# Optimization experiments

Measured on AMD Instinct MI355X. Metric: run time of the kernel, lower is better.

Reference implementation:

```python
import jax, jax.numpy as jnp
import numpy as np

HS = [192, 96, 48, 24, 12, 6]
WS = [384, 192, 96, 48, 24, 12]
C = 64    # feature channels per pyramid level
F = 64    # num_features (conv output channels)
CIN = 2 * C + 2  # current + warped + 2 flow channels = 130
N = 4


def dense_image_warp(image, flow):
    """tfa.image.dense_image_warp: warped[b,y,x] = bilinear(image[b, y - flow_y, x - flow_x]).
    Boundary handling matches tfa._interpolate_bilinear: floor indices clipped to
    [0, size-2], interpolation alphas clipped to [0, 1]."""
    n, h, w, _ = image.shape
    gy, gx = jnp.meshgrid(jnp.arange(h, dtype=flow.dtype),
                          jnp.arange(w, dtype=flow.dtype), indexing='ij')
    qy = gy[None] - flow[..., 0]          # [N,H,W] query rows
    qx = gx[None] - flow[..., 1]          # [N,H,W] query cols
    y0 = jnp.clip(jnp.floor(qy), 0, h - 2).astype(jnp.int32)
    x0 = jnp.clip(jnp.floor(qx), 0, w - 2).astype(jnp.int32)
    ay = jnp.clip(qy - y0.astype(flow.dtype), 0.0, 1.0)[..., None]
    ax = jnp.clip(qx - x0.astype(flow.dtype), 0.0, 1.0)[..., None]
    b = jnp.arange(n)[:, None, None]
    tl = image[b, y0, x0]
    tr = image[b, y0, x0 + 1]
    bl = image[b, y0 + 1, x0]
    br = image[b, y0 + 1, x0 + 1]
    top = tl + (tr - tl) * ax
    bot = bl + (br - bl) * ax
    return top + (bot - top) * ay


def separable_conv1x1(x, dw, pw, bias):
    # SeparableConv2D with 1x1 kernel: depthwise per-channel scale, then pointwise matmul.
    return jnp.einsum('nhwc,cf->nhwf', x * dw, pw) + bias


def _forward(xcs, xps, fls, dws, pws, bs):
    outs = []
    for i in range(6):
        # _warp: dense_image_warp(x_prev, -flow)
        warped = dense_image_warp(xps[i], -fls[i])
        x = jnp.concatenate([xcs[i], warped, fls[i]], axis=-1)  # [N,H,W,130]
        outs.append(separable_conv1x1(x, dws[i], pws[i], bs[i]))
    return tuple(outs)


def setup_inputs() -> dict:
    key = jax.random.key(0)
    d = {}
    for i in range(6):
        h, w = HS[i], WS[i]
        ks = jax.random.split(jax.random.fold_in(key, i), 6)
        d[f'xc{i}'] = jax.random.normal(ks[0], (N, h, w, C), jnp.float32)
        d[f'xp{i}'] = jax.random.normal(ks[1], (N, h, w, C), jnp.float32)
        d[f'fl{i}'] = jax.random.normal(ks[2], (N, h, w, 2), jnp.float32) * 2.0
        d[f'dw{i}'] = jax.random.normal(ks[3], (CIN,), jnp.float32) * 0.1
        d[f'pw{i}'] = jax.random.normal(ks[4], (CIN, F), jnp.float32) * 0.05
        d[f'bias{i}'] = jnp.zeros((F,), jnp.float32)
    return d


def reference(xc0, xc1, xc2, xc3, xc4, xc5,
              xp0, xp1, xp2, xp3, xp4, xp5,
              fl0, fl1, fl2, fl3, fl4, fl5,
              dw0, dw1, dw2, dw3, dw4, dw5,
              pw0, pw1, pw2, pw3, pw4, pw5,
              bias0, bias1, bias2, bias3, bias4, bias5):
    xcs = (xc0, xc1, xc2, xc3, xc4, xc5)
    xps = (xp0, xp1, xp2, xp3, xp4, xp5)
    fls = (fl0, fl1, fl2, fl3, fl4, fl5)
    dws = (dw0, dw1, dw2, dw3, dw4, dw5)
    pws = (pw0, pw1, pw2, pw3, pw4, pw5)
    bs = (bias0, bias1, bias2, bias3, bias4, bias5)
    return _forward(xcs, xps, fls, dws, pws, bs)
```

## Files before the change

kernel.cpp:

```cpp
#include <hip/hip_runtime.h>


typedef __attribute__((ext_vector_type(8))) short bf16x8;
typedef __attribute__((ext_vector_type(4))) float f32x4;

#define WS_LVL_STRIDE 17408

__device__ inline unsigned rne_bf16_bits(float f) {
  unsigned u = __builtin_bit_cast(unsigned, f);
  u += 0x7fffu + ((u >> 16) & 1u);
  return u >> 16;
}
__device__ inline int pack_bf16x2(float a, float b) {
  return (int)(rne_bf16_bits(a) | (rne_bf16_bits(b) << 16));
}

struct LevelArgs {
  const float* __restrict__ xc;
  const float* __restrict__ xp;
  const float* __restrict__ fl;
  float* __restrict__ out;
  const char* __restrict__ wsl;
  int H, W, npix, block_start;
};
struct KArgs { LevelArgs lv[6]; int total_blocks; };

struct PrepLevel {
  const float* __restrict__ dw;
  const float* __restrict__ pw;
  const float* __restrict__ bias;
  char* __restrict__ wsl;
};
struct PrepArgs { PrepLevel lv[6]; };

__global__ void prep_kernel(PrepArgs pa) {
  const PrepLevel P = pa.lv[blockIdx.x];
  int4* __restrict__ frag = (int4*)P.wsl;
  for (int e = (int)threadIdx.x; e < 1024; e += 256) {
    const int kt = e >> 8;
    const int nt = (e >> 6) & 3;
    const int lane = e & 63;
    const int n = nt * 16 + (lane & 15);
    const int kb = kt * 32 + ((lane >> 4) & 3) * 8;
    int v[4];
#pragma unroll
    for (int jj = 0; jj < 4; ++jj) {
      const int k0 = kb + jj * 2;
      const float w0 = P.dw[k0] * P.pw[(size_t)k0 * 64 + n];
      const float w1 = P.dw[k0 + 1] * P.pw[(size_t)(k0 + 1) * 64 + n];
      v[jj] = pack_bf16x2(w0, w1);
    }
    frag[e] = make_int4(v[0], v[1], v[2], v[3]);
  }
  float* __restrict__ tab = (float*)(P.wsl + 16384);
  if (threadIdx.x < 64) {
    const int f = (int)threadIdx.x;
    tab[f] = P.bias[f];
    tab[64 + f] = P.dw[128] * P.pw[128 * 64 + f];
    tab[128 + f] = P.dw[129] * P.pw[129 * 64 + f];
  }
}

#define LDS_ROW 144
#define LDS_FL_OFF (256 * LDS_ROW)

__global__ __launch_bounds__(256, 3) void flowwarp_mfma(KArgs ka) {
  __shared__ __align__(16) char lds_raw[256 * LDS_ROW + 256 * 8];

  const int nb = ka.total_blocks;
  const int chunk = (nb + 7) >> 3;
  const int bp = (int)blockIdx.x;
  const int b = (bp & 7) * chunk + (bp >> 3);
  if (b >= nb) return;

  int Lr = 0;
#pragma unroll
  for (int i = 1; i < 6; ++i) Lr = (b >= ka.lv[i].block_start) ? i : Lr;
  const int L = __builtin_amdgcn_readfirstlane(Lr);
  const LevelArgs A = ka.lv[L];

  const int q = (int)threadIdx.x;
  const int p0 = (b - A.block_start) * 256;
  const int W = A.W, H = A.H;

  {
    int p = p0 + q;
    if (p > A.npix - 1) p = A.npix - 1;
    const int x = p % W;
    const int t = p / W;
    const int y = t % H;
    const int n = t / H;

    const float fl0 = A.fl[2 * (size_t)p];
    const float fl1 = A.fl[2 * (size_t)p + 1];
    ((float2*)(lds_raw + LDS_FL_OFF))[q] = make_float2(fl0, fl1);

    const float qy = (float)y + fl0;
    const float qx = (float)x + fl1;
    const float fy = fminf(fmaxf(floorf(qy), 0.0f), (float)(H - 2));
    const float fx = fminf(fmaxf(floorf(qx), 0.0f), (float)(W - 2));
    const int y0 = (int)fy, x0 = (int)fx;
    const float ay = fminf(fmaxf(qy - fy, 0.0f), 1.0f);
    const float ax = fminf(fmaxf(qx - fx, 0.0f), 1.0f);

    const float* __restrict__ base =
        A.xp + ((size_t)((n * H + y0) * W + x0)) * 64;
    const int W64 = W * 64;
    const float4* __restrict__ tl4 = (const float4*)base;
    const float4* __restrict__ tr4 = (const float4*)(base + 64);
    const float4* __restrict__ bl4 = (const float4*)(base + W64);
    const float4* __restrict__ br4 = (const float4*)(base + W64 + 64);
    int4* __restrict__ xrow = (int4*)(lds_raw + (size_t)q * LDS_ROW);

#pragma unroll 1
    for (int bq = 0; bq < 4; ++bq) {
      float4 rtl[4], rtr[4], rbl[4], rbr[4];
#pragma unroll
      for (int i = 0; i < 4; ++i) {
        rtl[i] = tl4[bq * 4 + i];
        rtr[i] = tr4[bq * 4 + i];
        rbl[i] = bl4[bq * 4 + i];
        rbr[i] = br4[bq * 4 + i];
      }
      int v[8];
#pragma unroll
      for (int i = 0; i < 4; ++i) {
        const float atl[4] = {rtl[i].x, rtl[i].y, rtl[i].z, rtl[i].w};
        const float atr[4] = {rtr[i].x, rtr[i].y, rtr[i].z, rtr[i].w};
        const float abl[4] = {rbl[i].x, rbl[i].y, rbl[i].z, rbl[i].w};
        const float abr[4] = {rbr[i].x, rbr[i].y, rbr[i].z, rbr[i].w};
        float wv[4];
#pragma unroll
        for (int j = 0; j < 4; ++j) {
          const float top = fmaf(atr[j] - atl[j], ax, atl[j]);
          const float bot = fmaf(abr[j] - abl[j], ax, abl[j]);
          wv[j] = fmaf(bot - top, ay, top);
        }
        v[i * 2] = pack_bf16x2(wv[0], wv[1]);
        v[i * 2 + 1] = pack_bf16x2(wv[2], wv[3]);
      }
      xrow[bq * 2] = make_int4(v[0], v[1], v[2], v[3]);
      xrow[bq * 2 + 1] = make_int4(v[4], v[5], v[6], v[7]);
    }
  }
  __syncthreads();

  const int lane = q & 63;
  const int w = q >> 6;
  const int m16 = lane & 15;
  const int q4l = lane >> 4;

  const int4* __restrict__ bfr = (const int4*)A.wsl;
  bf16x8 Bf[4][4];
#pragma unroll
  for (int kt = 0; kt < 4; ++kt)
#pragma unroll
    for (int nt = 0; nt < 4; ++nt)
      Bf[kt][nt] = __builtin_bit_cast(bf16x8, bfr[(kt * 4 + nt) * 64 + lane]);

  const float* __restrict__ tab = (const float*)(A.wsl + 16384);
  float bv[4], t0v[4], t1v[4];
#pragma unroll
  for (int nt = 0; nt < 4; ++nt) {
    const int col = nt * 16 + m16;
    bv[nt] = tab[col];
    t0v[nt] = tab[64 + col];
    t1v[nt] = tab[128 + col];
  }
  const float2* __restrict__ flsh = (const float2*)(lds_raw + LDS_FL_OFF);

#pragma unroll 1
  for (int mt = 0; mt < 4; ++mt) {
    const int lrow = w * 64 + mt * 16;
    int pm = p0 + lrow + m16;
    if (pm > A.npix - 1) pm = A.npix - 1;
    const float* __restrict__ xcp = A.xc + (size_t)pm * 64 + q4l * 8;
    const float4 a0 = *(const float4*)xcp;
    const float4 a1 = *(const float4*)(xcp + 4);
    const float4 a2 = *(const float4*)(xcp + 32);
    const float4 a3 = *(const float4*)(xcp + 36);
    int av[8];
    av[0] = pack_bf16x2(a0.x, a0.y); av[1] = pack_bf16x2(a0.z, a0.w);
    av[2] = pack_bf16x2(a1.x, a1.y); av[3] = pack_bf16x2(a1.z, a1.w);
    av[4] = pack_bf16x2(a2.x, a2.y); av[5] = pack_bf16x2(a2.z, a2.w);
    av[6] = pack_bf16x2(a3.x, a3.y); av[7] = pack_bf16x2(a3.z, a3.w);
    const bf16x8 A0 = __builtin_bit_cast(bf16x8, make_int4(av[0], av[1], av[2], av[3]));
    const bf16x8 A1 = __builtin_bit_cast(bf16x8, make_int4(av[4], av[5], av[6], av[7]));
    const int4* __restrict__ lrp =
        (const int4*)(lds_raw + (size_t)(lrow + m16) * LDS_ROW + q4l * 16);
    const bf16x8 A2 = __builtin_bit_cast(bf16x8, lrp[0]);
    const bf16x8 A3 = __builtin_bit_cast(bf16x8, lrp[4]);

    f32x4 acc[4] = {{0.f, 0.f, 0.f, 0.f}, {0.f, 0.f, 0.f, 0.f},
                    {0.f, 0.f, 0.f, 0.f}, {0.f, 0.f, 0.f, 0.f}};
#pragma unroll
    for (int nt = 0; nt < 4; ++nt) {
      acc[nt] = __builtin_amdgcn_mfma_f32_16x16x32_bf16(A0, Bf[0][nt], acc[nt], 0, 0, 0);
      acc[nt] = __builtin_amdgcn_mfma_f32_16x16x32_bf16(A1, Bf[1][nt], acc[nt], 0, 0, 0);
      acc[nt] = __builtin_amdgcn_mfma_f32_16x16x32_bf16(A2, Bf[2][nt], acc[nt], 0, 0, 0);
      acc[nt] = __builtin_amdgcn_mfma_f32_16x16x32_bf16(A3, Bf[3][nt], acc[nt], 0, 0, 0);
    }

    float f0[4], f1[4];
#pragma unroll
    for (int i = 0; i < 4; ++i) {
      const float2 f = flsh[lrow + q4l * 4 + i];
      f0[i] = f.x; f1[i] = f.y;
    }
#pragma unroll
    for (int i = 0; i < 4; ++i) {
      const int prow = p0 + lrow + q4l * 4 + i;
      if (prow < A.npix) {
        float* __restrict__ orow = A.out + (size_t)prow * 64 + m16;
#pragma unroll
        for (int nt = 0; nt < 4; ++nt)
          orow[nt * 16] = acc[nt][i] + bv[nt] + f0[i] * t0v[nt] + f1[i] * t1v[nt];
      }
    }
  }
}

extern "C" void kernel_launch(void* const* d_in, const int* in_sizes, int n_in,
                              void* d_out, int out_size, void* d_ws, size_t ws_size,
                              hipStream_t stream) {
  static const int HS[6] = {192, 96, 48, 24, 12, 6};
  static const int WS[6] = {384, 192, 96, 48, 24, 12};
  PrepArgs pa;
  KArgs ka;
  int bstart = 0;
  size_t ooff = 0;
  for (int i = 0; i < 6; ++i) {
    char* wsl = (char*)d_ws + (size_t)i * WS_LVL_STRIDE;
    pa.lv[i].dw   = (const float*)d_in[6 * i + 3];
    pa.lv[i].pw   = (const float*)d_in[6 * i + 4];
    pa.lv[i].bias = (const float*)d_in[6 * i + 5];
    pa.lv[i].wsl  = wsl;
    ka.lv[i].xc  = (const float*)d_in[6 * i + 0];
    ka.lv[i].xp  = (const float*)d_in[6 * i + 1];
    ka.lv[i].fl  = (const float*)d_in[6 * i + 2];
    ka.lv[i].out = (float*)d_out + ooff;
    ka.lv[i].wsl = wsl;
    const int npix = 4 * HS[i] * WS[i];
    ka.lv[i].H = HS[i];
    ka.lv[i].W = WS[i];
    ka.lv[i].npix = npix;
    ka.lv[i].block_start = bstart;
    bstart += (npix + 255) / 256;
    ooff += (size_t)npix * 64;
  }
  ka.total_blocks = bstart;
  prep_kernel<<<dim3(6), dim3(256), 0, stream>>>(pa);
  const int chunk = (bstart + 7) >> 3;
  flowwarp_mfma<<<dim3(chunk * 8), dim3(256), 0, stream>>>(ka);
}
```

Before: 403.2 us.

## Shrink LDS with XOR-swizzled rows and reload flow from global to raise occupancy

Replaces the padded 144-byte LDS rows with dense 128-byte rows that use an XOR swizzle to avoid bank conflicts, and removes the LDS flow buffer by re-reading flow values from global memory in the epilogue. This cuts LDS per block from about 38KB to 32KB, and launch bounds are raised from 3 to 5 blocks per CU to allow more concurrent waves. The cost is extra global flow loads, which are likely cached, plus tighter register limits that could cause spills.

```diff
diff --git a/kernel.cpp b/kernel.cpp
--- a/kernel.cpp
+++ b/kernel.cpp
@@ -61,11 +61,11 @@
   }
 }
 
-#define LDS_ROW 144
-#define LDS_FL_OFF (256 * LDS_ROW)
-
-__global__ __launch_bounds__(256, 3) void flowwarp_mfma(KArgs ka) {
-  __shared__ __align__(16) char lds_raw[256 * LDS_ROW + 256 * 8];
+#define SWZ(r, o) \
+  ((((unsigned)(r)) << 7) | (((unsigned)(o)) ^ ((((unsigned)(r)) & 7u) << 4)))
+
+__global__ __launch_bounds__(256, 5) void flowwarp_mfma(KArgs ka) {
+  __shared__ __align__(16) char lds_raw[256 * 128];
 
   const int nb = ka.total_blocks;
   const int chunk = (nb + 7) >> 3;
@@ -93,7 +93,6 @@
 
     const float fl0 = A.fl[2 * (size_t)p];
     const float fl1 = A.fl[2 * (size_t)p + 1];
-    ((float2*)(lds_raw + LDS_FL_OFF))[q] = make_float2(fl0, fl1);
 
     const float qy = (float)y + fl0;
     const float qx = (float)x + fl1;
@@ -110,7 +109,6 @@
     const float4* __restrict__ tr4 = (const float4*)(base + 64);
     const float4* __restrict__ bl4 = (const float4*)(base + W64);
     const float4* __restrict__ br4 = (const float4*)(base + W64 + 64);
-    int4* __restrict__ xrow = (int4*)(lds_raw + (size_t)q * LDS_ROW);
 
 #pragma unroll 1
     for (int bq = 0; bq < 4; ++bq) {
@@ -139,8 +137,9 @@
         v[i * 2] = pack_bf16x2(wv[0], wv[1]);
         v[i * 2 + 1] = pack_bf16x2(wv[2], wv[3]);
       }
-      xrow[bq * 2] = make_int4(v[0], v[1], v[2], v[3]);
-      xrow[bq * 2 + 1] = make_int4(v[4], v[5], v[6], v[7]);
+      *(int4*)(lds_raw + SWZ(q, bq * 32)) = make_int4(v[0], v[1], v[2], v[3]);
+      *(int4*)(lds_raw + SWZ(q, bq * 32 + 16)) =
+          make_int4(v[4], v[5], v[6], v[7]);
     }
   }
   __syncthreads();
@@ -167,11 +166,18 @@
     t0v[nt] = tab[64 + col];
     t1v[nt] = tab[128 + col];
   }
-  const float2* __restrict__ flsh = (const float2*)(lds_raw + LDS_FL_OFF);
+  const float2* __restrict__ flg = (const float2*)A.fl;
 
 #pragma unroll 1
   for (int mt = 0; mt < 4; ++mt) {
     const int lrow = w * 64 + mt * 16;
+    float2 fle[4];
+#pragma unroll
+    for (int i = 0; i < 4; ++i) {
+      int pr = p0 + lrow + q4l * 4 + i;
+      if (pr > A.npix - 1) pr = A.npix - 1;
+      fle[i] = flg[pr];
+    }
     int pm = p0 + lrow + m16;
     if (pm > A.npix - 1) pm = A.npix - 1;
     const float* __restrict__ xcp = A.xc + (size_t)pm * 64 + q4l * 8;
@@ -186,10 +192,11 @@
     av[6] = pack_bf16x2(a3.x, a3.y); av[7] = pack_bf16x2(a3.z, a3.w);
     const bf16x8 A0 = __builtin_bit_cast(bf16x8, make_int4(av[0], av[1], av[2], av[3]));
     const bf16x8 A1 = __builtin_bit_cast(bf16x8, make_int4(av[4], av[5], av[6], av[7]));
-    const int4* __restrict__ lrp =
-        (const int4*)(lds_raw + (size_t)(lrow + m16) * LDS_ROW + q4l * 16);
-    const bf16x8 A2 = __builtin_bit_cast(bf16x8, lrp[0]);
-    const bf16x8 A3 = __builtin_bit_cast(bf16x8, lrp[4]);
+    const int rr = lrow + m16;
+    const bf16x8 A2 = __builtin_bit_cast(
+        bf16x8, *(const int4*)(lds_raw + SWZ(rr, q4l * 16)));
+    const bf16x8 A3 = __builtin_bit_cast(
+        bf16x8, *(const int4*)(lds_raw + SWZ(rr, 64 + q4l * 16)));
 
     f32x4 acc[4] = {{0.f, 0.f, 0.f, 0.f}, {0.f, 0.f, 0.f, 0.f},
                     {0.f, 0.f, 0.f, 0.f}, {0.f, 0.f, 0.f, 0.f}};
@@ -201,12 +208,6 @@
       acc[nt] = __builtin_amdgcn_mfma_f32_16x16x32_bf16(A3, Bf[3][nt], acc[nt], 0, 0, 0);
     }
 
-    float f0[4], f1[4];
-#pragma unroll
-    for (int i = 0; i < 4; ++i) {
-      const float2 f = flsh[lrow + q4l * 4 + i];
-      f0[i] = f.x; f1[i] = f.y;
-    }
 #pragma unroll
     for (int i = 0; i < 4; ++i) {
       const int prow = p0 + lrow + q4l * 4 + i;
@@ -214,7 +215,7 @@
         float* __restrict__ orow = A.out + (size_t)prow * 64 + m16;
 #pragma unroll
         for (int nt = 0; nt < 4; ++nt)
-          orow[nt * 16] = acc[nt][i] + bv[nt] + f0[i] * t0v[nt] + f1[i] * t1v[nt];
+          orow[nt * 16] = acc[nt][i] + bv[nt] + fle[i].x * t0v[nt] + fle[i].y * t1v[nt];
       }
     }
   }
```

Result: slower. 415.4 us (+3.0%).
